# Kernel tuning notes

Measured on AMD Instinct MI355X. Metric: run time of the kernel, lower is better.

The kernel has to match this reference:

```python
import jax, jax.numpy as jnp
import numpy as np

D_MODEL = 1024
NUM_HEADS = 16
D_K = D_MODEL // NUM_HEADS
B, S = 4, 2048


def setup_inputs() -> dict:
    key = jax.random.key(0)
    ks = jax.random.split(key, 11)
    scale = 1.0 / np.sqrt(D_MODEL)
    inp = {
        'query': jax.random.normal(ks[0], (B, S, D_MODEL), dtype=jnp.float32),
        'key':   jax.random.normal(ks[1], (B, S, D_MODEL), dtype=jnp.float32),
        'value': jax.random.normal(ks[2], (B, S, D_MODEL), dtype=jnp.float32),
        'Wq': jax.random.normal(ks[3], (D_MODEL, D_MODEL), dtype=jnp.float32) * scale,
        'bq': jnp.zeros((D_MODEL,), dtype=jnp.float32),
        'Wk': jax.random.normal(ks[4], (D_MODEL, D_MODEL), dtype=jnp.float32) * scale,
        'bk': jnp.zeros((D_MODEL,), dtype=jnp.float32),
        'Wv': jax.random.normal(ks[5], (D_MODEL, D_MODEL), dtype=jnp.float32) * scale,
        'bv': jnp.zeros((D_MODEL,), dtype=jnp.float32),
        'Wo': jax.random.normal(ks[6], (D_MODEL, D_MODEL), dtype=jnp.float32) * scale,
        'bo': jnp.zeros((D_MODEL,), dtype=jnp.float32),
    }
    return inp


def reference(query, key, value, Wq, bq, Wk, bk, Wv, bv, Wo, bo):
    b, sq, _ = query.shape
    sk = key.shape[1]
    # projections (torch Linear: x @ W.T + b; here W stored as [in, out])
    Q = query @ Wq + bq
    K = key @ Wk + bk
    V = value @ Wv + bv
    # split heads: [b, h, s, d_k]
    Q = Q.reshape(b, sq, NUM_HEADS, D_K).transpose(0, 2, 1, 3)
    K = K.reshape(b, sk, NUM_HEADS, D_K).transpose(0, 2, 1, 3)
    V = V.reshape(b, sk, NUM_HEADS, D_K).transpose(0, 2, 1, 3)
    # scaled dot-product attention (full [b,h,sq,sk] scores, as in source)
    scores = jnp.einsum('bhqd,bhkd->bhqk', Q, K) / jnp.sqrt(jnp.float32(D_K))
    attn = jax.nn.softmax(scores, axis=-1)
    out = jnp.einsum('bhqk,bhkd->bhqd', attn, V)
    out = out.transpose(0, 2, 1, 3).reshape(b, sq, D_MODEL)
    return out @ Wo + bo
```

## Files before the change

kernel.cpp:

```cpp
#include <hip/hip_runtime.h>
#include <hip/hip_bf16.h>
#include <stdint.h>

typedef __bf16 bf16x8 __attribute__((ext_vector_type(8)));
typedef __bf16 bf16x4 __attribute__((ext_vector_type(4)));
typedef float  f32x4  __attribute__((ext_vector_type(4)));
typedef unsigned short u16;

#define D_MODEL 1024
#define NUM_HEADS 16
#define DK 64
#define BATCH 4
#define SEQ 2048
#define M_TOTAL (BATCH*SEQ)
#define MD ((size_t)M_TOTAL * D_MODEL)
#define QK_SCALE 0.18033688011112042f

static __device__ __forceinline__ u16 f2bf(float f) {
    __bf16 h = (__bf16)f;
    return __builtin_bit_cast(u16, h);
}

#define ASYNC16(gptr, lptr) __builtin_amdgcn_global_load_lds( \
    (const __attribute__((address_space(1))) unsigned*)(uintptr_t)(gptr), \
    (__attribute__((address_space(3))) unsigned*)(unsigned)(uintptr_t)(lptr), 16, 0, 0)

__global__ __launch_bounds__(256) void prep(
    const u16* __restrict__ q, const u16* __restrict__ k, const u16* __restrict__ v,
    const u16* __restrict__ W0, const u16* __restrict__ W1,
    const u16* __restrict__ W2, const u16* __restrict__ W3,
    u16* __restrict__ WT, u16* __restrict__ CVT, unsigned* __restrict__ flagp)
{
    __shared__ u16 tile[32][33];
    __shared__ int cnts[4];
    const int tid = threadIdx.x;
    const int lane = tid & 63, w = tid >> 6;

    {
        u16 s = q[2 * tid];
        int e = (s >> 7) & 0xFF;
        unsigned long long m = __ballot(e >= 100 && e <= 134);
        if (lane == 0) cnts[w] = __popcll(m);
    }
    __syncthreads();
    const bool is_bf16 = (cnts[0] + cnts[1] + cnts[2] + cnts[3]) > 128;
    if (blockIdx.x == 0 && tid == 0) *flagp = is_bf16 ? 1u : 0u;

    const int id = blockIdx.x;
    if (id < 4096) {
        const int z   = id >> 10;
        const int rem = id & 1023;
        const int bx = (rem & 31) * 32, by = (rem >> 5) * 32;
        const u16* W = (z == 0) ? W0 : (z == 1) ? W1 : (z == 2) ? W2 : W3;
        u16* T = WT + (size_t)z * D_MODEL * D_MODEL;
        const int x = tid & 31, y0 = tid >> 5;
        if (is_bf16) {
#pragma unroll
            for (int i = 0; i < 4; i++) {
                int y = y0 + i * 8;
                tile[y][x] = W[(size_t)(by + y) * D_MODEL + bx + x];
            }
        } else {
            const float* Wf = (const float*)W;
#pragma unroll
            for (int i = 0; i < 4; i++) {
                int y = y0 + i * 8;
                tile[y][x] = f2bf(Wf[(size_t)(by + y) * D_MODEL + bx + x]);
            }
        }
        __syncthreads();
#pragma unroll
        for (int i = 0; i < 4; i++) {
            int y = y0 + i * 8;
            T[(size_t)(bx + y) * D_MODEL + by + x] = tile[x][y];
        }
    } else {
        if (is_bf16) return;
        const int cid = id - 4096;
        const size_t stride = (size_t)2048 * 256 * 8;
        const float* srcs[3] = { (const float*)q, (const float*)k, (const float*)v };
        for (size_t idx = ((size_t)cid * 256 + tid) * 8; idx < 3 * MD; idx += stride) {
            const int z = (int)(idx >> 23);
            const size_t off = idx & (MD - 1);
            const float* src = srcs[z];
            float4 f0 = *(const float4*)(src + off);
            float4 f1 = *(const float4*)(src + off + 4);
            bf16x8 p;
            p[0] = (__bf16)f0.x; p[1] = (__bf16)f0.y; p[2] = (__bf16)f0.z; p[3] = (__bf16)f0.w;
            p[4] = (__bf16)f1.x; p[5] = (__bf16)f1.y; p[6] = (__bf16)f1.z; p[7] = (__bf16)f1.w;
            *(bf16x8*)(CVT + (size_t)z * MD + off) = p;
        }
    }
}

__global__ __launch_bounds__(256) void gemm_qkv(
    const u16* __restrict__ qin, const u16* __restrict__ kin, const u16* __restrict__ vin,
    const u16* __restrict__ CVT, const u16* __restrict__ WT,
    const u16* __restrict__ bq, const u16* __restrict__ bk, const u16* __restrict__ bv,
    u16* __restrict__ Qp, u16* __restrict__ Kp, u16* __restrict__ VpT,
    const unsigned* __restrict__ flagp)
{
    __shared__ __align__(16) u16 As[128 * 64];
    __shared__ __align__(16) u16 Bs[128 * 64];

    const int id  = blockIdx.x;
    const int wg  = (id & 7) * 192 + (id >> 3);
    const int z   = wg >> 9;
    const int rr  = wg & 511;
    const int m_blk = (rr >> 3) * 128;
    const int n_blk = (rr & 7) * 128;

    const bool is_bf16 = (*flagp != 0);
    const u16* A = is_bf16 ? ((z == 0) ? qin : (z == 1) ? kin : vin)
                           : (CVT + (size_t)z * MD);
    const u16* W    = WT + (size_t)z * 1048576;
    const u16* bias = (z == 0) ? bq : (z == 1) ? bk : bv;
    u16* C          = (z == 0) ? Qp : (z == 1) ? Kp : VpT;
    const float oscale = (z == 0) ? QK_SCALE : 1.0f;

    const int tid  = threadIdx.x;
    const int lane = tid & 63, w = tid >> 6;
    const int quad = lane >> 4, l15 = lane & 15;
    const int swz  = l15 & 7;
    const int wm = w >> 1, wn = w & 1;

    const int lrow = lane >> 3;
    const int ug   = (lane & 7) ^ lrow;

    f32x4 acc[4][4] = {};

    for (int k0 = 0; k0 < D_MODEL; k0 += 64) {
#pragma unroll
        for (int i = 0; i < 4; i++) {
            const int c = w * 4 + i;
            ASYNC16(A + (size_t)(m_blk + c * 8 + lrow) * D_MODEL + k0 + ug * 8, &As[c * 512]);
            ASYNC16(W + (size_t)(n_blk + c * 8 + lrow) * D_MODEL + k0 + ug * 8, &Bs[c * 512]);
        }
        __syncthreads();

        bf16x8 a[4][2], b[4][2];
#pragma unroll
        for (int mf = 0; mf < 4; mf++)
#pragma unroll
            for (int ks = 0; ks < 2; ks++)
                a[mf][ks] = *(const bf16x8*)&As[(size_t)(wm * 64 + mf * 16 + l15) * 64
                                                + (((ks * 4 + quad) ^ swz) * 8)];
#pragma unroll
        for (int nf = 0; nf < 4; nf++)
#pragma unroll
            for (int ks = 0; ks < 2; ks++)
                b[nf][ks] = *(const bf16x8*)&Bs[(size_t)(wn * 64 + nf * 16 + l15) * 64
                                                + (((ks * 4 + quad) ^ swz) * 8)];
#pragma unroll
        for (int mf = 0; mf < 4; mf++)
#pragma unroll
            for (int nf = 0; nf < 4; nf++)
#pragma unroll
                for (int ks = 0; ks < 2; ks++)
                    acc[mf][nf] = __builtin_amdgcn_mfma_f32_16x16x32_bf16(
                        a[mf][ks], b[nf][ks], acc[mf][nf], 0, 0, 0);
        __syncthreads();
    }

#pragma unroll
    for (int nf = 0; nf < 4; nf++) {
        const int n = n_blk + wn * 64 + nf * 16 + l15;
        const float bvf = is_bf16 ? (float)((const __bf16*)bias)[n] : ((const float*)bias)[n];
#pragma unroll
        for (int mf = 0; mf < 4; mf++) {
            const int mrow = m_blk + wm * 64 + mf * 16 + quad * 4;
            if (z == 2) {
                const int bb = mrow >> 11, s = mrow & 2047;
                ushort4 pk;
                pk.x = f2bf(acc[mf][nf][0] + bvf);
                pk.y = f2bf(acc[mf][nf][1] + bvf);
                pk.z = f2bf(acc[mf][nf][2] + bvf);
                pk.w = f2bf(acc[mf][nf][3] + bvf);
                *(ushort4*)(C + (size_t)bb * D_MODEL * SEQ + (size_t)n * SEQ + s) = pk;
            } else {
#pragma unroll
                for (int r = 0; r < 4; r++)
                    C[(size_t)(mrow + r) * D_MODEL + n] = f2bf((acc[mf][nf][r] + bvf) * oscale);
            }
        }
    }
}

__global__ __launch_bounds__(256) void gemm_o(
    const u16* __restrict__ A, const u16* __restrict__ WT,
    const u16* __restrict__ bias, u16* __restrict__ C,
    const unsigned* __restrict__ flagp)
{
    __shared__ __align__(16) u16 As[128 * 64];
    __shared__ __align__(16) u16 Bs[128 * 64];

    const int id  = blockIdx.x;
    const int wg  = (id & 7) * 64 + (id >> 3);
    const int m_blk = (wg >> 3) * 128;
    const int n_blk = (wg & 7) * 128;

    const bool is_bf16 = (*flagp != 0);

    const int tid  = threadIdx.x;
    const int lane = tid & 63, w = tid >> 6;
    const int quad = lane >> 4, l15 = lane & 15;
    const int swz  = l15 & 7;
    const int wm = w >> 1, wn = w & 1;

    const int lrow = lane >> 3;
    const int ug   = (lane & 7) ^ lrow;

    f32x4 acc[4][4] = {};

    for (int k0 = 0; k0 < D_MODEL; k0 += 64) {
#pragma unroll
        for (int i = 0; i < 4; i++) {
            const int c = w * 4 + i;
            ASYNC16(A  + (size_t)(m_blk + c * 8 + lrow) * D_MODEL + k0 + ug * 8, &As[c * 512]);
            ASYNC16(WT + (size_t)(n_blk + c * 8 + lrow) * D_MODEL + k0 + ug * 8, &Bs[c * 512]);
        }
        __syncthreads();

        bf16x8 a[4][2], b[4][2];
#pragma unroll
        for (int mf = 0; mf < 4; mf++)
#pragma unroll
            for (int ks = 0; ks < 2; ks++)
                a[mf][ks] = *(const bf16x8*)&As[(size_t)(wm * 64 + mf * 16 + l15) * 64
                                                + (((ks * 4 + quad) ^ swz) * 8)];
#pragma unroll
        for (int nf = 0; nf < 4; nf++)
#pragma unroll
            for (int ks = 0; ks < 2; ks++)
                b[nf][ks] = *(const bf16x8*)&Bs[(size_t)(wn * 64 + nf * 16 + l15) * 64
                                                + (((ks * 4 + quad) ^ swz) * 8)];
#pragma unroll
        for (int mf = 0; mf < 4; mf++)
#pragma unroll
            for (int nf = 0; nf < 4; nf++)
#pragma unroll
                for (int ks = 0; ks < 2; ks++)
                    acc[mf][nf] = __builtin_amdgcn_mfma_f32_16x16x32_bf16(
                        a[mf][ks], b[nf][ks], acc[mf][nf], 0, 0, 0);
        __syncthreads();
    }

#pragma unroll
    for (int nf = 0; nf < 4; nf++) {
        const int n = n_blk + wn * 64 + nf * 16 + l15;
        const float bvf = is_bf16 ? (float)((const __bf16*)bias)[n] : ((const float*)bias)[n];
#pragma unroll
        for (int mf = 0; mf < 4; mf++) {
            const int mrow = m_blk + wm * 64 + mf * 16 + quad * 4;
            if (!is_bf16) {
                float* Cf = (float*)C;
#pragma unroll
                for (int r = 0; r < 4; r++)
                    Cf[(size_t)(mrow + r) * D_MODEL + n] = acc[mf][nf][r] + bvf;
            } else {
#pragma unroll
                for (int r = 0; r < 4; r++)
                    C[(size_t)(mrow + r) * D_MODEL + n] = f2bf(acc[mf][nf][r] + bvf);
            }
        }
    }
}

__global__ __launch_bounds__(512, 4) void attn_kernel(
    const u16* __restrict__ Qp, const u16* __restrict__ Kp,
    const u16* __restrict__ VpT, u16* __restrict__ AO)
{
    __shared__ __align__(16) u16 Ks[2][64 * 64];
    __shared__ __align__(16) u16 Vs[2][64 * 64];
    __shared__ __align__(16) u16 Ps[8][32][68];
    const int id  = blockIdx.x;
    const int xcd = id & 7, j = id >> 3;
    const int bh  = xcd * 8 + (j >> 3);
    const int qx  = j & 7;

    const int tid  = threadIdx.x;
    const int lane = tid & 63, w = tid >> 6;
    const int quad = lane >> 4, l15 = lane & 15;
    const int b = bh >> 4, h = bh & 15;
    const int q_base = qx * 256 + w * 32;

    bf16x8 bQ[2][2];
#pragma unroll
    for (int sn = 0; sn < 2; sn++)
#pragma unroll
        for (int ds = 0; ds < 2; ds++)
            bQ[sn][ds] = *(const bf16x8*)(Qp + (size_t)(b * SEQ + q_base + sn * 16 + l15) * D_MODEL
                                              + h * DK + ds * 32 + quad * 8);

    f32x4 OT[2][4] = {};
    f32x4 OTs[2]  = {};
    bf16x8 aOnes;
#pragma unroll
    for (int i = 0; i < 8; i++) aOnes[i] = (__bf16)1.0f;

    const u16* Kbase = Kp  + (size_t)(b * SEQ) * D_MODEL + h * DK;
    const u16* Vbase = VpT + (size_t)b * D_MODEL * SEQ + (size_t)(h * DK) * SEQ;

    const int lrow = lane >> 3;
    const int ug   = (lane & 7) ^ lrow;
    const int swz  = l15 & 7;

    auto issue_tile = [&](int key0, int bf) {
        ASYNC16(Kbase + (size_t)(key0 + w * 8 + lrow) * D_MODEL + ug * 8, &Ks[bf][w * 512]);
        ASYNC16(Vbase + (size_t)(w * 8 + lrow) * SEQ + key0 + ug * 8,     &Vs[bf][w * 512]);
    };

    issue_tile(0, 0);
    __syncthreads();

    for (int t = 0; t < SEQ / 64; t++) {
        const int cur = t & 1;
        if (t + 1 < SEQ / 64) issue_tile((t + 1) * 64, cur ^ 1);

#pragma unroll
        for (int kc = 0; kc < 4; kc++) {
            const int krow = (kc * 16 + l15) * 64;
            bf16x8 k0 = *(const bf16x8*)&Ks[cur][krow + ((quad ^ swz) * 8)];
            bf16x8 k1 = *(const bf16x8*)&Ks[cur][krow + (((4 + quad) ^ swz) * 8)];
#pragma unroll
            for (int sn = 0; sn < 2; sn++) {
                f32x4 s = {};
                __builtin_amdgcn_s_setprio(1);
                s = __builtin_amdgcn_mfma_f32_16x16x32_bf16(k0, bQ[sn][0], s, 0, 0, 0);
                s = __builtin_amdgcn_mfma_f32_16x16x32_bf16(k1, bQ[sn][1], s, 0, 0, 0);
                __builtin_amdgcn_s_setprio(0);
                bf16x4 pk;
                pk[0] = (__bf16)__builtin_amdgcn_exp2f(s[0]);
                pk[1] = (__bf16)__builtin_amdgcn_exp2f(s[1]);
                pk[2] = (__bf16)__builtin_amdgcn_exp2f(s[2]);
                pk[3] = (__bf16)__builtin_amdgcn_exp2f(s[3]);
                *(bf16x4*)&Ps[w][sn * 16 + l15][kc * 16 + quad * 4] = pk;
            }
        }

#pragma unroll
        for (int kc2 = 0; kc2 < 2; kc2++) {
            bf16x8 bP0 = *(const bf16x8*)&Ps[w][l15][kc2 * 32 + quad * 8];
            bf16x8 bP1 = *(const bf16x8*)&Ps[w][16 + l15][kc2 * 32 + quad * 8];
            __builtin_amdgcn_s_setprio(1);
            OTs[0] = __builtin_amdgcn_mfma_f32_16x16x32_bf16(aOnes, bP0, OTs[0], 0, 0, 0);
            OTs[1] = __builtin_amdgcn_mfma_f32_16x16x32_bf16(aOnes, bP1, OTs[1], 0, 0, 0);
#pragma unroll
            for (int nd = 0; nd < 4; nd++) {
                bf16x8 aV = *(const bf16x8*)&Vs[cur][(nd * 16 + l15) * 64
                                                    + (((kc2 * 4 + quad) ^ swz) * 8)];
                OT[0][nd] = __builtin_amdgcn_mfma_f32_16x16x32_bf16(aV, bP0, OT[0][nd], 0, 0, 0);
                OT[1][nd] = __builtin_amdgcn_mfma_f32_16x16x32_bf16(aV, bP1, OT[1][nd], 0, 0, 0);
            }
            __builtin_amdgcn_s_setprio(0);
        }
        __syncthreads();
    }

#pragma unroll
    for (int sn = 0; sn < 2; sn++) {
        float rl = 1.0f / OTs[sn][0];
        size_t rowbase = (size_t)(b * SEQ + q_base + sn * 16 + l15) * D_MODEL + h * DK;
#pragma unroll
        for (int nd = 0; nd < 4; nd++) {
            ushort4 pk;
            pk.x = f2bf(OT[sn][nd][0] * rl);
            pk.y = f2bf(OT[sn][nd][1] * rl);
            pk.z = f2bf(OT[sn][nd][2] * rl);
            pk.w = f2bf(OT[sn][nd][3] * rl);
            *(ushort4*)(AO + rowbase + nd * 16 + quad * 4) = pk;
        }
    }
}

extern "C" void kernel_launch(void* const* d_in, const int* in_sizes, int n_in,
                              void* d_out, int out_size, void* d_ws, size_t ws_size,
                              hipStream_t stream) {
    const u16* q  = (const u16*)d_in[0];
    const u16* k  = (const u16*)d_in[1];
    const u16* v  = (const u16*)d_in[2];
    const u16* Wq = (const u16*)d_in[3];
    const u16* bq = (const u16*)d_in[4];
    const u16* Wk = (const u16*)d_in[5];
    const u16* bk = (const u16*)d_in[6];
    const u16* Wv = (const u16*)d_in[7];
    const u16* bv = (const u16*)d_in[8];
    const u16* Wo = (const u16*)d_in[9];
    const u16* bo = (const u16*)d_in[10];

    u16* ws   = (u16*)d_ws;
    unsigned* flagp = (unsigned*)ws;
    u16* WT   = ws + 16;
    u16* Qp   = WT + (size_t)4 * 1024 * 1024;
    u16* Kp   = Qp + MD;
    u16* VpT  = Kp + MD;
    u16* CVT  = VpT + MD;
    u16* AO   = CVT;

    prep<<<6144, 256, 0, stream>>>(q, k, v, Wq, Wk, Wv, Wo, WT, CVT, flagp);
    gemm_qkv<<<1536, 256, 0, stream>>>(q, k, v, CVT, WT, bq, bk, bv, Qp, Kp, VpT, flagp);
    attn_kernel<<<512, 512, 0, stream>>>(Qp, Kp, VpT, AO);
    gemm_o<<<512, 256, 0, stream>>>(AO, WT + 3 * 1048576, bo, (u16*)d_out, flagp);
}
```

Baseline: 356.5 us.

## Fuse fp32-to-bf16 input conversion into QKV GEMM tile loads

Drops the separate pass in the prep kernel that converted the fp32 query/key/value inputs to bf16 in a workspace buffer. The QKV GEMM now async-loads fp32 A tiles straight into a larger shared buffer with an XOR swizzle and converts them to bf16 in registers before the MFMAs. This avoids writing and re-reading the converted activations in global memory. In exchange, each GEMM k-step loads twice as many A bytes into LDS, uses more shared memory (which may lower occupancy), and adds conversion instructions. The A-tiles are re-read across 8 N-blocks per M-block, so more total fp32 traffic hits the caches.

```diff
diff --git a/kernel.cpp b/kernel.cpp
--- a/kernel.cpp
+++ b/kernel.cpp
@@ -26,10 +26,10 @@
     (__attribute__((address_space(3))) unsigned*)(unsigned)(uintptr_t)(lptr), 16, 0, 0)
 
 __global__ __launch_bounds__(256) void prep(
-    const u16* __restrict__ q, const u16* __restrict__ k, const u16* __restrict__ v,
+    const u16* __restrict__ q,
     const u16* __restrict__ W0, const u16* __restrict__ W1,
     const u16* __restrict__ W2, const u16* __restrict__ W3,
-    u16* __restrict__ WT, u16* __restrict__ CVT, unsigned* __restrict__ flagp)
+    u16* __restrict__ WT, unsigned* __restrict__ flagp)
 {
     __shared__ u16 tile[32][33];
     __shared__ int cnts[4];
@@ -46,62 +46,45 @@
     const bool is_bf16 = (cnts[0] + cnts[1] + cnts[2] + cnts[3]) > 128;
     if (blockIdx.x == 0 && tid == 0) *flagp = is_bf16 ? 1u : 0u;
 
-    const int id = blockIdx.x;
-    if (id < 4096) {
-        const int z   = id >> 10;
-        const int rem = id & 1023;
-        const int bx = (rem & 31) * 32, by = (rem >> 5) * 32;
-        const u16* W = (z == 0) ? W0 : (z == 1) ? W1 : (z == 2) ? W2 : W3;
-        u16* T = WT + (size_t)z * D_MODEL * D_MODEL;
-        const int x = tid & 31, y0 = tid >> 5;
-        if (is_bf16) {
-#pragma unroll
-            for (int i = 0; i < 4; i++) {
-                int y = y0 + i * 8;
-                tile[y][x] = W[(size_t)(by + y) * D_MODEL + bx + x];
-            }
-        } else {
-            const float* Wf = (const float*)W;
-#pragma unroll
-            for (int i = 0; i < 4; i++) {
-                int y = y0 + i * 8;
-                tile[y][x] = f2bf(Wf[(size_t)(by + y) * D_MODEL + bx + x]);
-            }
-        }
-        __syncthreads();
+    const int id  = blockIdx.x;
+    const int z   = id >> 10;
+    const int rem = id & 1023;
+    const int bx = (rem & 31) * 32, by = (rem >> 5) * 32;
+    const u16* W = (z == 0) ? W0 : (z == 1) ? W1 : (z == 2) ? W2 : W3;
+    u16* T = WT + (size_t)z * D_MODEL * D_MODEL;
+    const int x = tid & 31, y0 = tid >> 5;
+    if (is_bf16) {
 #pragma unroll
         for (int i = 0; i < 4; i++) {
             int y = y0 + i * 8;
-            T[(size_t)(bx + y) * D_MODEL + by + x] = tile[x][y];
+            tile[y][x] = W[(size_t)(by + y) * D_MODEL + bx + x];
         }
     } else {
-        if (is_bf16) return;
-        const int cid = id - 4096;
-        const size_t stride = (size_t)2048 * 256 * 8;
-        const float* srcs[3] = { (const float*)q, (const float*)k, (const float*)v };
-        for (size_t idx = ((size_t)cid * 256 + tid) * 8; idx < 3 * MD; idx += stride) {
-            const int z = (int)(idx >> 23);
-            const size_t off = idx & (MD - 1);
-            const float* src = srcs[z];
-            float4 f0 = *(const float4*)(src + off);
-            float4 f1 = *(const float4*)(src + off + 4);
-            bf16x8 p;
-            p[0] = (__bf16)f0.x; p[1] = (__bf16)f0.y; p[2] = (__bf16)f0.z; p[3] = (__bf16)f0.w;
-            p[4] = (__bf16)f1.x; p[5] = (__bf16)f1.y; p[6] = (__bf16)f1.z; p[7] = (__bf16)f1.w;
-            *(bf16x8*)(CVT + (size_t)z * MD + off) = p;
-        }
+        const float* Wf = (const float*)W;
+#pragma unroll
+        for (int i = 0; i < 4; i++) {
+            int y = y0 + i * 8;
+            tile[y][x] = f2bf(Wf[(size_t)(by + y) * D_MODEL + bx + x]);
+        }
+    }
+    __syncthreads();
+#pragma unroll
+    for (int i = 0; i < 4; i++) {
+        int y = y0 + i * 8;
+        T[(size_t)(bx + y) * D_MODEL + by + x] = tile[x][y];
     }
 }
 
 __global__ __launch_bounds__(256) void gemm_qkv(
     const u16* __restrict__ qin, const u16* __restrict__ kin, const u16* __restrict__ vin,
-    const u16* __restrict__ CVT, const u16* __restrict__ WT,
+    const u16* __restrict__ WT,
     const u16* __restrict__ bq, const u16* __restrict__ bk, const u16* __restrict__ bv,
     u16* __restrict__ Qp, u16* __restrict__ Kp, u16* __restrict__ VpT,
     const unsigned* __restrict__ flagp)
 {
-    __shared__ __align__(16) u16 As[128 * 64];
-    __shared__ __align__(16) u16 Bs[128 * 64];
+    __shared__ __align__(16) float Asf[128 * 64];
+    __shared__ __align__(16) u16  Bs[128 * 64];
+    u16* Asb = (u16*)Asf;
 
     const int id  = blockIdx.x;
     const int wg  = (id & 7) * 192 + (id >> 3);
@@ -111,8 +94,8 @@
     const int n_blk = (rr & 7) * 128;
 
     const bool is_bf16 = (*flagp != 0);
-    const u16* A = is_bf16 ? ((z == 0) ? qin : (z == 1) ? kin : vin)
-                           : (CVT + (size_t)z * MD);
+    const u16* A    = (z == 0) ? qin : (z == 1) ? kin : vin;
+    const float* Af = (const float*)A;
     const u16* W    = WT + (size_t)z * 1048576;
     const u16* bias = (z == 0) ? bq : (z == 1) ? bk : bv;
     u16* C          = (z == 0) ? Qp : (z == 1) ? Kp : VpT;
@@ -126,25 +109,59 @@
 
     const int lrow = lane >> 3;
     const int ug   = (lane & 7) ^ lrow;
+    const int lrow2 = lane >> 4;
+    const int p16   = lane & 15;
 
     f32x4 acc[4][4] = {};
 
     for (int k0 = 0; k0 < D_MODEL; k0 += 64) {
+        if (is_bf16) {
+#pragma unroll
+            for (int i = 0; i < 4; i++) {
+                const int c = w * 4 + i;
+                ASYNC16(A + (size_t)(m_blk + c * 8 + lrow) * D_MODEL + k0 + ug * 8, Asb + c * 512);
+            }
+        } else {
+#pragma unroll
+            for (int i = 0; i < 8; i++) {
+                const int c   = w * 8 + i;
+                const int row = c * 4 + lrow2;
+                const int g   = p16 ^ ((row & 7) << 1);
+                ASYNC16(Af + (size_t)(m_blk + row) * D_MODEL + k0 + g * 4, Asb + c * 512);
+            }
+        }
 #pragma unroll
         for (int i = 0; i < 4; i++) {
             const int c = w * 4 + i;
-            ASYNC16(A + (size_t)(m_blk + c * 8 + lrow) * D_MODEL + k0 + ug * 8, &As[c * 512]);
             ASYNC16(W + (size_t)(n_blk + c * 8 + lrow) * D_MODEL + k0 + ug * 8, &Bs[c * 512]);
         }
         __syncthreads();
 
         bf16x8 a[4][2], b[4][2];
-#pragma unroll
-        for (int mf = 0; mf < 4; mf++)
-#pragma unroll
-            for (int ks = 0; ks < 2; ks++)
-                a[mf][ks] = *(const bf16x8*)&As[(size_t)(wm * 64 + mf * 16 + l15) * 64
-                                                + (((ks * 4 + quad) ^ swz) * 8)];
+        if (is_bf16) {
+#pragma unroll
+            for (int mf = 0; mf < 4; mf++)
+#pragma unroll
+                for (int ks = 0; ks < 2; ks++)
+                    a[mf][ks] = *(const bf16x8*)&Asb[(size_t)(wm * 64 + mf * 16 + l15) * 64
+                                                     + (((ks * 4 + quad) ^ swz) * 8)];
+        } else {
+#pragma unroll
+            for (int mf = 0; mf < 4; mf++)
+#pragma unroll
+                for (int ks = 0; ks < 2; ks++) {
+                    const int roff = (wm * 64 + mf * 16 + l15) * 64;
+                    const int fo   = ((ks * 4 + quad) ^ swz) * 8;
+                    f32x4 lo = *(const f32x4*)&Asf[roff + fo];
+                    f32x4 hi = *(const f32x4*)&Asf[roff + fo + 4];
+                    bf16x8 p;
+                    p[0] = (__bf16)lo[0]; p[1] = (__bf16)lo[1];
+                    p[2] = (__bf16)lo[2]; p[3] = (__bf16)lo[3];
+                    p[4] = (__bf16)hi[0]; p[5] = (__bf16)hi[1];
+                    p[6] = (__bf16)hi[2]; p[7] = (__bf16)hi[3];
+                    a[mf][ks] = p;
+                }
+        }
 #pragma unroll
         for (int nf = 0; nf < 4; nf++)
 #pragma unroll
@@ -394,11 +411,10 @@
     u16* Qp   = WT + (size_t)4 * 1024 * 1024;
     u16* Kp   = Qp + MD;
     u16* VpT  = Kp + MD;
-    u16* CVT  = VpT + MD;
-    u16* AO   = CVT;
-
-    prep<<<6144, 256, 0, stream>>>(q, k, v, Wq, Wk, Wv, Wo, WT, CVT, flagp);
-    gemm_qkv<<<1536, 256, 0, stream>>>(q, k, v, CVT, WT, bq, bk, bv, Qp, Kp, VpT, flagp);
+    u16* AO   = VpT + MD;
+
+    prep<<<4096, 256, 0, stream>>>(q, Wq, Wk, Wv, Wo, WT, flagp);
+    gemm_qkv<<<1536, 256, 0, stream>>>(q, k, v, WT, bq, bk, bv, Qp, Kp, VpT, flagp);
     attn_kernel<<<512, 512, 0, stream>>>(Qp, Kp, VpT, AO);
     gemm_o<<<512, 256, 0, stream>>>(AO, WT + 3 * 1048576, bo, (u16*)d_out, flagp);
 }
```

After: 362.9 us. About the same (+1.8%).
